# Optimization experiments

Measured on AMD Instinct MI355X. Metric: run time of the kernel, lower is better.

## Reference

```python
import jax, jax.numpy as jnp
import numpy as np

SEQ_LENGTH = 1000
NUM_FEATURES = 5
HIDDEN = 128


def setup_inputs() -> dict:
    key = jax.random.key(0)
    ks = jax.random.split(key, 12)
    k = 1.0 / np.sqrt(HIDDEN)  # torch default uniform bound
    # recurrence stays numerically bounded; math is identical.
    u = lambda kk, shape, s=k: jax.random.uniform(kk, shape, jnp.float32, -s, s)
    return {
        "x": jax.random.normal(ks[0], (256, 800, NUM_FEATURES), jnp.float32),
        "h_state": jnp.zeros((2, 256, HIDDEN), jnp.float32),
        "w_ih0": u(ks[1], (HIDDEN, NUM_FEATURES)),
        "w_hh0": u(ks[2], (HIDDEN, HIDDEN), 0.5 * k),
        "b_ih0": u(ks[3], (HIDDEN,)),
        "b_hh0": u(ks[4], (HIDDEN,)),
        "w_ih1": u(ks[5], (HIDDEN, HIDDEN), 0.5 * k),
        "w_hh1": u(ks[6], (HIDDEN, HIDDEN), 0.5 * k),
        "b_ih1": u(ks[7], (HIDDEN,)),
        "b_hh1": u(ks[8], (HIDDEN,)),
        "w_out": u(ks[9], (1, HIDDEN)),
        "b_out": u(ks[10], (1,)),
    }


def reference(x, h_state, w_ih0, w_hh0, b_ih0, b_hh0,
              w_ih1, w_hh1, b_ih1, b_hh1, w_out, b_out):
    B, T_in, F = x.shape
    # pad time dim to SEQ_LENGTH with zeros (torch.cat with delta)
    pad = jnp.zeros((B, SEQ_LENGTH - T_in, F), x.dtype)
    xp = jnp.concatenate([x, pad], axis=1)  # [B, 1000, F]
    xs = jnp.swapaxes(xp, 0, 1)  # [T, B, F] for scan

    def step(carry, x_t):
        h0, h1 = carry
        h0 = jax.nn.relu(x_t @ w_ih0.T + b_ih0 + h0 @ w_hh0.T + b_hh0)
        h1 = jax.nn.relu(h0 @ w_ih1.T + b_ih1 + h1 @ w_hh1.T + b_hh1)
        return (h0, h1), h1

    (h0f, h1f), ys = jax.lax.scan(step, (h_state[0], h_state[1]), xs)
    r_out = jnp.swapaxes(ys, 0, 1)  # [B, 1000, H]
    out = jax.nn.sigmoid(r_out @ w_out.T + b_out)  # [B, 1000, 1]
    return out[:, :T_in], jnp.stack([h0f, h1f])
```

## Files before the change

### kernel.cpp

```cpp
#include <hip/hip_runtime.h>
#include <math.h>


#define TT    1000
#define TIN   800
#define HD    128
#define NF    5
#define BATCH 256
#define RS    136
#define AS    132
#define SK1   20
#define NSTEP (TT + SK1)

typedef _Float16 h16x2 __attribute__((ext_vector_type(2)));
typedef _Float16 h16x8 __attribute__((ext_vector_type(8)));
typedef float    f32x4 __attribute__((ext_vector_type(4)));

template<int CTRL>
__device__ __forceinline__ float dpp_mov(float v) {
    union { float f; int i; } u, r;
    u.f = v;
    r.i = __builtin_amdgcn_update_dpp(0, u.i, CTRL, 0xF, 0xF, true);
    return r.f;
}

__global__ __launch_bounds__(512, 2) void rnn_dec(
    const float* __restrict__ x,
    const float* __restrict__ h_state,
    const float* __restrict__ w_ih0,
    const float* __restrict__ w_hh0,
    const float* __restrict__ b_ih0,
    const float* __restrict__ b_hh0,
    const float* __restrict__ w_ih1,
    const float* __restrict__ w_hh1,
    const float* __restrict__ b_ih1,
    const float* __restrict__ b_hh1,
    const float* __restrict__ w_out,
    const float* __restrict__ b_out,
    float* __restrict__ out)
{
    __shared__ __align__(16) _Float16 x_h[TIN * 8];
    __shared__ __align__(16) _Float16 ring0[32][RS];
    __shared__ __align__(16) _Float16 ring1[32][RS];
    __shared__ __align__(16) float    A_f[32][AS];
    __shared__ float y_lds[TIN];

    const int tid  = threadIdx.x;
    const int bb   = blockIdx.x;
    const int wv   = tid >> 6;
    const int lane = tid & 63;

    for (int i = tid; i < TIN * 8; i += 512) x_h[i] = (_Float16)0.f;
    __syncthreads();
    for (int i = tid; i < TIN * NF; i += 512) {
        int t = i / 5, f = i - 5 * t;
        x_h[t * 8 + f] = (_Float16)x[bb * (TIN * NF) + i];
    }
    if (tid < HD) {
        ring0[31][tid] = (_Float16)h_state[bb * HD + tid];
        ring1[31][tid] = (_Float16)h_state[BATCH * HD + bb * HD + tid];
    }

    const int c    = lane & 3;
    const int rg   = lane >> 2;
    const int g    = 2 * (c & 1) + ((c >> 1) & 1);
    const int half = wv & 1;
    const int row  = half * 64 + rg * 4 + g;

    union WU {
        h16x2 wp[4][16];
        h16x8 af[4][4];
        h16x2 wo[16];
    } W;

    float bias = 0.f;
    h16x2 wx[3];
    if (wv < 4) {
        const float* Wsrc = (wv < 2) ? w_hh0 : w_hh1;
        #pragma unroll
        for (int j = 0; j < 4; ++j) {
            const float* rp = Wsrc + (half * 64 + rg * 4 + (j ^ g)) * HD + c * 32;
            #pragma unroll
            for (int t = 0; t < 16; ++t) {
                h16x2 w2 = { (_Float16)rp[2 * t], (_Float16)rp[2 * t + 1] };
                W.wp[j][t] = w2;
            }
        }
        if (wv < 2) {
            wx[0][0] = (_Float16)w_ih0[row * NF + 0];
            wx[0][1] = (_Float16)w_ih0[row * NF + 1];
            wx[1][0] = (_Float16)w_ih0[row * NF + 2];
            wx[1][1] = (_Float16)w_ih0[row * NF + 3];
            wx[2][0] = (_Float16)w_ih0[row * NF + 4];
            wx[2][1] = (_Float16)0.f;
            bias = b_ih0[row] + b_hh0[row];
        } else {
            bias = b_ih1[row] + b_hh1[row];
        }
    } else if (wv < 6) {
        const int m0 = (wv - 4) * 64;
        #pragma unroll
        for (int mt = 0; mt < 4; ++mt) {
            #pragma unroll
            for (int kt = 0; kt < 4; ++kt) {
                const float* rp = w_ih1 + (m0 + mt * 16 + (lane & 15)) * HD
                                + kt * 32 + (lane >> 4) * 8;
                h16x8 v;
                #pragma unroll
                for (int j = 0; j < 8; ++j) v[j] = (_Float16)rp[j];
                W.af[mt][kt] = v;
            }
        }
    } else if (wv == 6) {
        const int c4 = lane & 3;
        #pragma unroll
        for (int t = 0; t < 16; ++t) {
            h16x2 w2 = { (_Float16)w_out[c4 * 32 + 2 * t],
                         (_Float16)w_out[c4 * 32 + 2 * t + 1] };
            W.wo[t] = w2;
        }
    }
    const float bout = b_out[0];

    float hfin = 0.f;

    __syncthreads();

    auto matvec = [&](const _Float16* base) -> float {
        h16x8 hv[4];
        #pragma unroll
        for (int u2 = 0; u2 < 4; ++u2)
            hv[u2] = *(const h16x8*)(base + c * 32 + 8 * u2);
        float a[4] = {0.f, 0.f, 0.f, 0.f};
        #pragma unroll
        for (int j = 0; j < 4; ++j) {
            float aj = 0.f;
            #pragma unroll
            for (int t = 0; t < 16; ++t) {
                h16x2 hp = { hv[t >> 2][2 * (t & 3)], hv[t >> 2][2 * (t & 3) + 1] };
                aj = __builtin_amdgcn_fdot2(W.wp[j][t], hp, aj, false);
            }
            a[j] = aj;
        }
        a[0] += dpp_mov<0xB1>(a[2]);
        a[1] += dpp_mov<0xB1>(a[3]);
        a[0] += dpp_mov<0x4E>(a[1]);
        return a[0];
    };

    for (int s = 0; s < NSTEP; ++s) {
        if (wv < 2) {
            if (s < TT) {
                float v = matvec(&ring0[(s + 31) & 31][0]) + bias;
                if (s < TIN) {
                    h16x8 xv = *(const h16x8*)(&x_h[s * 8]);
                    h16x2 xp0 = { xv[0], xv[1] };
                    h16x2 xp1 = { xv[2], xv[3] };
                    h16x2 xp2 = { xv[4], xv[5] };
                    float xc = __builtin_amdgcn_fdot2(wx[2], xp2, 0.f, false);
                    xc = __builtin_amdgcn_fdot2(wx[1], xp1, xc, false);
                    xc = __builtin_amdgcn_fdot2(wx[0], xp0, xc, false);
                    v += xc;
                }
                v = fmaxf(v, 0.f);
                ring0[s & 31][row] = (_Float16)v;
                if (s == TT - 1) hfin = v;
            }
        } else if (wv < 4) {
            if (s >= SK1) {
                const int u = s - SK1;
                float v = matvec(&ring1[(u + 31) & 31][0]);
                v = fmaxf(v + bias + A_f[u & 31][row], 0.f);
                ring1[u & 31][row] = (_Float16)v;
                if (u == TT - 1) hfin = v;
            }
        } else if (wv < 6) {
            if (s >= 17 && s <= 1009 && ((s - 17) & 15) == 0) {
                const int ub = s - 17;
                const int un = ub + (lane & 15);
                h16x8 bf[4];
                #pragma unroll
                for (int kt = 0; kt < 4; ++kt)
                    bf[kt] = *(const h16x8*)(&ring0[un & 31]
                                             [kt * 32 + (lane >> 4) * 8]);
                #pragma unroll
                for (int mt = 0; mt < 4; ++mt) {
                    f32x4 acc = {0.f, 0.f, 0.f, 0.f};
                    #pragma unroll
                    for (int kt = 0; kt < 4; ++kt)
                        acc = __builtin_amdgcn_mfma_f32_16x16x32_f16(
                            W.af[mt][kt], bf[kt], acc, 0, 0, 0);
                    if (un < TT)
                        *(f32x4*)(&A_f[un & 31]
                                  [(wv - 4) * 64 + mt * 16 + (lane >> 4) * 4]) = acc;
                }
            }
        } else if (wv == 6) {
            if (s >= 37 && s <= 821 && ((s - 37) & 15) == 0) {
                const int slot = lane >> 2;
                const int c4   = lane & 3;
                const int t    = (s - 37) + slot;
                const _Float16* rb = &ring1[t & 31][0] + c4 * 32;
                float z = 0.f;
                #pragma unroll
                for (int u2 = 0; u2 < 4; ++u2) {
                    h16x8 hv = *(const h16x8*)(rb + 8 * u2);
                    h16x2 hp0 = { hv[0], hv[1] };
                    h16x2 hp1 = { hv[2], hv[3] };
                    h16x2 hp2 = { hv[4], hv[5] };
                    h16x2 hp3 = { hv[6], hv[7] };
                    z = __builtin_amdgcn_fdot2(W.wo[4 * u2 + 0], hp0, z, false);
                    z = __builtin_amdgcn_fdot2(W.wo[4 * u2 + 1], hp1, z, false);
                    z = __builtin_amdgcn_fdot2(W.wo[4 * u2 + 2], hp2, z, false);
                    z = __builtin_amdgcn_fdot2(W.wo[4 * u2 + 3], hp3, z, false);
                }
                z += dpp_mov<0xB1>(z);
                z += dpp_mov<0x4E>(z);
                if (c4 == 0) y_lds[t] = 1.f / (1.f + expf(-(z + bout)));
            }
        }
        __syncthreads();
    }

    for (int i = tid; i < TIN; i += 512)
        out[bb * TIN + i] = y_lds[i];
    if (wv < 2)
        out[TIN * BATCH + bb * HD + row] = hfin;
    else if (wv < 4)
        out[TIN * BATCH + BATCH * HD + bb * HD + row] = hfin;
}

extern "C" void kernel_launch(void* const* d_in, const int* in_sizes, int n_in,
                              void* d_out, int out_size, void* d_ws, size_t ws_size,
                              hipStream_t stream) {
    (void)in_sizes; (void)n_in; (void)d_ws; (void)ws_size; (void)out_size;
    rnn_dec<<<dim3(BATCH), dim3(512), 0, stream>>>(
        (const float*)d_in[0],  (const float*)d_in[1],
        (const float*)d_in[2],  (const float*)d_in[3],
        (const float*)d_in[4],  (const float*)d_in[5],
        (const float*)d_in[6],  (const float*)d_in[7],
        (const float*)d_in[8],  (const float*)d_in[9],
        (const float*)d_in[10], (const float*)d_in[11],
        (float*)d_out);
}
```

Measured before the change: 429.4 us.

## Halve block to four waves, one per layer, with two steps per barrier

The block shrinks from 512 to 256 threads. Each recurrent layer is now handled by a single wave, with every lane computing two hidden rows over a 64-wide slice, and the MFMA and output-projection waves are merged into the remaining two. The time loop runs two recurrence steps between barriers, relying on in-order LDS access within a wave, to cut barrier count and cross-wave reduction shuffles. In exchange, each step's serial dot-product chain per wave doubles, the wave-level parallelism per CU drops, and the looser synchronisation narrows the margin on ring-buffer reuse.

```diff
diff --git a/kernel.cpp b/kernel.cpp
--- a/kernel.cpp
+++ b/kernel.cpp
@@ -24,7 +24,7 @@
     return r.f;
 }
 
-__global__ __launch_bounds__(512, 2) void rnn_dec(
+__global__ __launch_bounds__(256, 1) void rnn_sc(
     const float* __restrict__ x,
     const float* __restrict__ h_state,
     const float* __restrict__ w_ih0,
@@ -50,9 +50,9 @@
     const int wv   = tid >> 6;
     const int lane = tid & 63;
 
-    for (int i = tid; i < TIN * 8; i += 512) x_h[i] = (_Float16)0.f;
+    for (int i = tid; i < TIN * 8; i += 256) x_h[i] = (_Float16)0.f;
     __syncthreads();
-    for (int i = tid; i < TIN * NF; i += 512) {
+    for (int i = tid; i < TIN * NF; i += 256) {
         int t = i / 5, f = i - 5 * t;
         x_h[t * 8 + f] = (_Float16)x[bb * (TIN * NF) + i];
     }
@@ -61,44 +61,48 @@
         ring1[31][tid] = (_Float16)h_state[BATCH * HD + bb * HD + tid];
     }
 
-    const int c    = lane & 3;
-    const int rg   = lane >> 2;
-    const int g    = 2 * (c & 1) + ((c >> 1) & 1);
-    const int half = wv & 1;
-    const int row  = half * 64 + rg * 4 + g;
+    const int c      = lane & 1;
+    const int rg     = lane >> 1;
+    const int g2     = 2 * c;
+    const int base_r = rg * 4 + 2 * c;
 
     union WU {
-        h16x2 wp[4][16];
+        h16x2 wp[4][32];
         h16x8 af[4][4];
-        h16x2 wo[16];
     } W;
-
-    float bias = 0.f;
-    h16x2 wx[3];
-    if (wv < 4) {
-        const float* Wsrc = (wv < 2) ? w_hh0 : w_hh1;
+    h16x2 wo[16];
+    h16x2 wxa[3], wxb[3];
+    float bias0 = 0.f, bias1 = 0.f;
+
+    if (wv < 2) {
+        const float* Wsrc = (wv == 0) ? w_hh0 : w_hh1;
         #pragma unroll
         for (int j = 0; j < 4; ++j) {
-            const float* rp = Wsrc + (half * 64 + rg * 4 + (j ^ g)) * HD + c * 32;
-            #pragma unroll
-            for (int t = 0; t < 16; ++t) {
+            const float* rp = Wsrc + (rg * 4 + (j ^ g2)) * HD + c * 64;
+            #pragma unroll
+            for (int t = 0; t < 32; ++t) {
                 h16x2 w2 = { (_Float16)rp[2 * t], (_Float16)rp[2 * t + 1] };
                 W.wp[j][t] = w2;
             }
         }
-        if (wv < 2) {
-            wx[0][0] = (_Float16)w_ih0[row * NF + 0];
-            wx[0][1] = (_Float16)w_ih0[row * NF + 1];
-            wx[1][0] = (_Float16)w_ih0[row * NF + 2];
-            wx[1][1] = (_Float16)w_ih0[row * NF + 3];
-            wx[2][0] = (_Float16)w_ih0[row * NF + 4];
-            wx[2][1] = (_Float16)0.f;
-            bias = b_ih0[row] + b_hh0[row];
+        if (wv == 0) {
+            #pragma unroll
+            for (int k = 0; k < 3; ++k) {
+                _Float16 a0 = (_Float16)w_ih0[base_r * NF + 2 * k];
+                _Float16 a1 = (2 * k + 1 < NF) ? (_Float16)w_ih0[base_r * NF + 2 * k + 1] : (_Float16)0.f;
+                _Float16 b0 = (_Float16)w_ih0[(base_r + 1) * NF + 2 * k];
+                _Float16 b1 = (2 * k + 1 < NF) ? (_Float16)w_ih0[(base_r + 1) * NF + 2 * k + 1] : (_Float16)0.f;
+                h16x2 wa = { a0, a1 }; wxa[k] = wa;
+                h16x2 wb = { b0, b1 }; wxb[k] = wb;
+            }
+            bias0 = b_ih0[base_r] + b_hh0[base_r];
+            bias1 = b_ih0[base_r + 1] + b_hh0[base_r + 1];
         } else {
-            bias = b_ih1[row] + b_hh1[row];
-        }
-    } else if (wv < 6) {
-        const int m0 = (wv - 4) * 64;
+            bias0 = b_ih1[base_r] + b_hh1[base_r];
+            bias1 = b_ih1[base_r + 1] + b_hh1[base_r + 1];
+        }
+    } else {
+        const int m0 = (wv == 2) ? 0 : 64;
         #pragma unroll
         for (int mt = 0; mt < 4; ++mt) {
             #pragma unroll
@@ -111,32 +115,33 @@
                 W.af[mt][kt] = v;
             }
         }
-    } else if (wv == 6) {
-        const int c4 = lane & 3;
-        #pragma unroll
-        for (int t = 0; t < 16; ++t) {
-            h16x2 w2 = { (_Float16)w_out[c4 * 32 + 2 * t],
-                         (_Float16)w_out[c4 * 32 + 2 * t + 1] };
-            W.wo[t] = w2;
+        if (wv == 3) {
+            const int c4 = lane & 3;
+            #pragma unroll
+            for (int t = 0; t < 16; ++t) {
+                h16x2 w2 = { (_Float16)w_out[c4 * 32 + 2 * t],
+                             (_Float16)w_out[c4 * 32 + 2 * t + 1] };
+                wo[t] = w2;
+            }
         }
     }
     const float bout = b_out[0];
 
-    float hfin = 0.f;
+    float hfin0 = 0.f, hfin1 = 0.f;
 
     __syncthreads();
 
-    auto matvec = [&](const _Float16* base) -> float {
-        h16x8 hv[4];
-        #pragma unroll
-        for (int u2 = 0; u2 < 4; ++u2)
-            hv[u2] = *(const h16x8*)(base + c * 32 + 8 * u2);
+    auto matvec = [&](const _Float16* base, float& r0, float& r1) {
+        h16x8 hv[8];
+        #pragma unroll
+        for (int u2 = 0; u2 < 8; ++u2)
+            hv[u2] = *(const h16x8*)(base + c * 64 + 8 * u2);
         float a[4] = {0.f, 0.f, 0.f, 0.f};
         #pragma unroll
         for (int j = 0; j < 4; ++j) {
             float aj = 0.f;
             #pragma unroll
-            for (int t = 0; t < 16; ++t) {
+            for (int t = 0; t < 32; ++t) {
                 h16x2 hp = { hv[t >> 2][2 * (t & 3)], hv[t >> 2][2 * (t & 3) + 1] };
                 aj = __builtin_amdgcn_fdot2(W.wp[j][t], hp, aj, false);
             }
@@ -144,38 +149,50 @@
         }
         a[0] += dpp_mov<0xB1>(a[2]);
         a[1] += dpp_mov<0xB1>(a[3]);
-        a[0] += dpp_mov<0x4E>(a[1]);
-        return a[0];
+        r0 = a[0];
+        r1 = a[1];
     };
 
-    for (int s = 0; s < NSTEP; ++s) {
-        if (wv < 2) {
+    auto body = [&](int s) {
+        if (wv == 0) {
             if (s < TT) {
-                float v = matvec(&ring0[(s + 31) & 31][0]) + bias;
+                float v0, v1;
+                matvec(&ring0[(s + 31) & 31][0], v0, v1);
+                v0 += bias0; v1 += bias1;
                 if (s < TIN) {
                     h16x8 xv = *(const h16x8*)(&x_h[s * 8]);
                     h16x2 xp0 = { xv[0], xv[1] };
                     h16x2 xp1 = { xv[2], xv[3] };
                     h16x2 xp2 = { xv[4], xv[5] };
-                    float xc = __builtin_amdgcn_fdot2(wx[2], xp2, 0.f, false);
-                    xc = __builtin_amdgcn_fdot2(wx[1], xp1, xc, false);
-                    xc = __builtin_amdgcn_fdot2(wx[0], xp0, xc, false);
-                    v += xc;
+                    float xc0 = __builtin_amdgcn_fdot2(wxa[2], xp2, 0.f, false);
+                    xc0 = __builtin_amdgcn_fdot2(wxa[1], xp1, xc0, false);
+                    xc0 = __builtin_amdgcn_fdot2(wxa[0], xp0, xc0, false);
+                    float xc1 = __builtin_amdgcn_fdot2(wxb[2], xp2, 0.f, false);
+                    xc1 = __builtin_amdgcn_fdot2(wxb[1], xp1, xc1, false);
+                    xc1 = __builtin_amdgcn_fdot2(wxb[0], xp0, xc1, false);
+                    v0 += xc0; v1 += xc1;
                 }
-                v = fmaxf(v, 0.f);
-                ring0[s & 31][row] = (_Float16)v;
-                if (s == TT - 1) hfin = v;
-            }
-        } else if (wv < 4) {
+                v0 = fmaxf(v0, 0.f);
+                v1 = fmaxf(v1, 0.f);
+                h16x2 hv = { (_Float16)v0, (_Float16)v1 };
+                *(h16x2*)(&ring0[s & 31][base_r]) = hv;
+                if (s == TT - 1) { hfin0 = v0; hfin1 = v1; }
+            }
+        } else if (wv == 1) {
             if (s >= SK1) {
                 const int u = s - SK1;
-                float v = matvec(&ring1[(u + 31) & 31][0]);
-                v = fmaxf(v + bias + A_f[u & 31][row], 0.f);
-                ring1[u & 31][row] = (_Float16)v;
-                if (u == TT - 1) hfin = v;
-            }
-        } else if (wv < 6) {
+                float v0, v1;
+                matvec(&ring1[(u + 31) & 31][0], v0, v1);
+                float2 av = *(const float2*)(&A_f[u & 31][base_r]);
+                v0 = fmaxf(v0 + bias0 + av.x, 0.f);
+                v1 = fmaxf(v1 + bias1 + av.y, 0.f);
+                h16x2 hv = { (_Float16)v0, (_Float16)v1 };
+                *(h16x2*)(&ring1[u & 31][base_r]) = hv;
+                if (u == TT - 1) { hfin0 = v0; hfin1 = v1; }
+            }
+        } else {
             if (s >= 17 && s <= 1009 && ((s - 17) & 15) == 0) {
+                const int m0 = (wv == 2) ? 0 : 64;
                 const int ub = s - 17;
                 const int un = ub + (lane & 15);
                 h16x8 bf[4];
@@ -192,11 +209,10 @@
                             W.af[mt][kt], bf[kt], acc, 0, 0, 0);
                     if (un < TT)
                         *(f32x4*)(&A_f[un & 31]
-                                  [(wv - 4) * 64 + mt * 16 + (lane >> 4) * 4]) = acc;
+                                  [m0 + mt * 16 + (lane >> 4) * 4]) = acc;
                 }
             }
-        } else if (wv == 6) {
-            if (s >= 37 && s <= 821 && ((s - 37) & 15) == 0) {
+            if (wv == 3 && s >= 37 && s <= 821 && ((s - 37) & 15) == 0) {
                 const int slot = lane >> 2;
                 const int c4   = lane & 3;
                 const int t    = (s - 37) + slot;
@@ -209,32 +225,37 @@
                     h16x2 hp1 = { hv[2], hv[3] };
                     h16x2 hp2 = { hv[4], hv[5] };
                     h16x2 hp3 = { hv[6], hv[7] };
-                    z = __builtin_amdgcn_fdot2(W.wo[4 * u2 + 0], hp0, z, false);
-                    z = __builtin_amdgcn_fdot2(W.wo[4 * u2 + 1], hp1, z, false);
-                    z = __builtin_amdgcn_fdot2(W.wo[4 * u2 + 2], hp2, z, false);
-                    z = __builtin_amdgcn_fdot2(W.wo[4 * u2 + 3], hp3, z, false);
+                    z = __builtin_amdgcn_fdot2(wo[4 * u2 + 0], hp0, z, false);
+                    z = __builtin_amdgcn_fdot2(wo[4 * u2 + 1], hp1, z, false);
+                    z = __builtin_amdgcn_fdot2(wo[4 * u2 + 2], hp2, z, false);
+                    z = __builtin_amdgcn_fdot2(wo[4 * u2 + 3], hp3, z, false);
                 }
                 z += dpp_mov<0xB1>(z);
                 z += dpp_mov<0x4E>(z);
                 if (c4 == 0) y_lds[t] = 1.f / (1.f + expf(-(z + bout)));
             }
         }
+    };
+
+    for (int s2 = 0; s2 < NSTEP; s2 += 2) {
+        body(s2);
+        body(s2 + 1);
         __syncthreads();
     }
 
-    for (int i = tid; i < TIN; i += 512)
+    for (int i = tid; i < TIN; i += 256)
         out[bb * TIN + i] = y_lds[i];
-    if (wv < 2)
-        out[TIN * BATCH + bb * HD + row] = hfin;
-    else if (wv < 4)
-        out[TIN * BATCH + BATCH * HD + bb * HD + row] = hfin;
+    if (wv == 0)
+        *(float2*)(&out[TIN * BATCH + bb * HD + base_r]) = make_float2(hfin0, hfin1);
+    else if (wv == 1)
+        *(float2*)(&out[TIN * BATCH + BATCH * HD + bb * HD + base_r]) = make_float2(hfin0, hfin1);
 }
 
 extern "C" void kernel_launch(void* const* d_in, const int* in_sizes, int n_in,
                               void* d_out, int out_size, void* d_ws, size_t ws_size,
                               hipStream_t stream) {
     (void)in_sizes; (void)n_in; (void)d_ws; (void)ws_size; (void)out_size;
-    rnn_dec<<<dim3(BATCH), dim3(512), 0, stream>>>(
+    rnn_sc<<<dim3(BATCH), dim3(256), 0, stream>>>(
         (const float*)d_in[0],  (const float*)d_in[1],
         (const float*)d_in[2],  (const float*)d_in[3],
         (const float*)d_in[4],  (const float*)d_in[5],
```

After: 517.3 us. +20.5%, slower.

## Shrink block to six waves and precompute layer-0 input projection in bursts

Applied to the files above, without the earlier changes.

Block size drops from eight waves to six (one idle wave was already unused). The output-projection work moves onto MFMA wave 4, and wave 5 computes the layer-0 input contribution for 16 timesteps at a time into a new LDS ring. Layer-0 waves then do a single LDS read on the critical path instead of three fdot2 ops. The per-step barrier involves fewer waves, which should cut sync cost. The trade-offs are extra LDS, more work on the MFMA waves, and a launch bound of one block per SIMD set.

```diff
diff --git a/kernel.cpp b/kernel.cpp
--- a/kernel.cpp
+++ b/kernel.cpp
@@ -24,7 +24,7 @@
     return r.f;
 }
 
-__global__ __launch_bounds__(512, 2) void rnn_dec(
+__global__ __launch_bounds__(384, 1) void rnn_c6(
     const float* __restrict__ x,
     const float* __restrict__ h_state,
     const float* __restrict__ w_ih0,
@@ -43,6 +43,7 @@
     __shared__ __align__(16) _Float16 ring0[32][RS];
     __shared__ __align__(16) _Float16 ring1[32][RS];
     __shared__ __align__(16) float    A_f[32][AS];
+    __shared__ __align__(16) float    xc_f[32][AS];
     __shared__ float y_lds[TIN];
 
     const int tid  = threadIdx.x;
@@ -50,9 +51,9 @@
     const int wv   = tid >> 6;
     const int lane = tid & 63;
 
-    for (int i = tid; i < TIN * 8; i += 512) x_h[i] = (_Float16)0.f;
+    for (int i = tid; i < TIN * 8; i += 384) x_h[i] = (_Float16)0.f;
     __syncthreads();
-    for (int i = tid; i < TIN * NF; i += 512) {
+    for (int i = tid; i < TIN * NF; i += 384) {
         int t = i / 5, f = i - 5 * t;
         x_h[t * 8 + f] = (_Float16)x[bb * (TIN * NF) + i];
     }
@@ -70,11 +71,11 @@
     union WU {
         h16x2 wp[4][16];
         h16x8 af[4][4];
-        h16x2 wo[16];
     } W;
-
+    h16x2 wo[16];
+    h16x2 xwa[3], xwb[3];
     float bias = 0.f;
-    h16x2 wx[3];
+
     if (wv < 4) {
         const float* Wsrc = (wv < 2) ? w_hh0 : w_hh1;
         #pragma unroll
@@ -86,19 +87,10 @@
                 W.wp[j][t] = w2;
             }
         }
-        if (wv < 2) {
-            wx[0][0] = (_Float16)w_ih0[row * NF + 0];
-            wx[0][1] = (_Float16)w_ih0[row * NF + 1];
-            wx[1][0] = (_Float16)w_ih0[row * NF + 2];
-            wx[1][1] = (_Float16)w_ih0[row * NF + 3];
-            wx[2][0] = (_Float16)w_ih0[row * NF + 4];
-            wx[2][1] = (_Float16)0.f;
-            bias = b_ih0[row] + b_hh0[row];
-        } else {
-            bias = b_ih1[row] + b_hh1[row];
-        }
-    } else if (wv < 6) {
-        const int m0 = (wv - 4) * 64;
+        bias = (wv < 2) ? (b_ih0[row] + b_hh0[row])
+                        : (b_ih1[row] + b_hh1[row]);
+    } else {
+        const int m0 = (wv == 4) ? 0 : 64;
         #pragma unroll
         for (int mt = 0; mt < 4; ++mt) {
             #pragma unroll
@@ -111,19 +103,51 @@
                 W.af[mt][kt] = v;
             }
         }
-    } else if (wv == 6) {
-        const int c4 = lane & 3;
-        #pragma unroll
-        for (int t = 0; t < 16; ++t) {
-            h16x2 w2 = { (_Float16)w_out[c4 * 32 + 2 * t],
-                         (_Float16)w_out[c4 * 32 + 2 * t + 1] };
-            W.wo[t] = w2;
+        if (wv == 4) {
+            const int c4 = lane & 3;
+            #pragma unroll
+            for (int t = 0; t < 16; ++t) {
+                h16x2 w2 = { (_Float16)w_out[c4 * 32 + 2 * t],
+                             (_Float16)w_out[c4 * 32 + 2 * t + 1] };
+                wo[t] = w2;
+            }
+        } else {
+            #pragma unroll
+            for (int k = 0; k < 3; ++k) {
+                _Float16 a0 = (_Float16)w_ih0[(2 * lane) * NF + 2 * k];
+                _Float16 a1 = (2 * k + 1 < NF) ? (_Float16)w_ih0[(2 * lane) * NF + 2 * k + 1] : (_Float16)0.f;
+                _Float16 b0 = (_Float16)w_ih0[(2 * lane + 1) * NF + 2 * k];
+                _Float16 b1 = (2 * k + 1 < NF) ? (_Float16)w_ih0[(2 * lane + 1) * NF + 2 * k + 1] : (_Float16)0.f;
+                h16x2 wa = { a0, a1 }; xwa[k] = wa;
+                h16x2 wb = { b0, b1 }; xwb[k] = wb;
+            }
         }
     }
     const float bout = b_out[0];
 
     float hfin = 0.f;
 
+    __syncthreads();
+
+    auto xc_burst = [&](int tb) {
+        #pragma unroll
+        for (int ti = 0; ti < 16; ++ti) {
+            const int t = tb + ti;
+            h16x8 xv = *(const h16x8*)(&x_h[t * 8]);
+            h16x2 xp0 = { xv[0], xv[1] };
+            h16x2 xp1 = { xv[2], xv[3] };
+            h16x2 xp2 = { xv[4], xv[5] };
+            float c0 = __builtin_amdgcn_fdot2(xwa[2], xp2, 0.f, false);
+            c0 = __builtin_amdgcn_fdot2(xwa[1], xp1, c0, false);
+            c0 = __builtin_amdgcn_fdot2(xwa[0], xp0, c0, false);
+            float c1 = __builtin_amdgcn_fdot2(xwb[2], xp2, 0.f, false);
+            c1 = __builtin_amdgcn_fdot2(xwb[1], xp1, c1, false);
+            c1 = __builtin_amdgcn_fdot2(xwb[0], xp0, c1, false);
+            *(float2*)(&xc_f[t & 31][2 * lane]) = make_float2(c0, c1);
+        }
+    };
+
+    if (wv == 5) xc_burst(0);
     __syncthreads();
 
     auto matvec = [&](const _Float16* base) -> float {
@@ -152,16 +176,7 @@
         if (wv < 2) {
             if (s < TT) {
                 float v = matvec(&ring0[(s + 31) & 31][0]) + bias;
-                if (s < TIN) {
-                    h16x8 xv = *(const h16x8*)(&x_h[s * 8]);
-                    h16x2 xp0 = { xv[0], xv[1] };
-                    h16x2 xp1 = { xv[2], xv[3] };
-                    h16x2 xp2 = { xv[4], xv[5] };
-                    float xc = __builtin_amdgcn_fdot2(wx[2], xp2, 0.f, false);
-                    xc = __builtin_amdgcn_fdot2(wx[1], xp1, xc, false);
-                    xc = __builtin_amdgcn_fdot2(wx[0], xp0, xc, false);
-                    v += xc;
-                }
+                if (s < TIN) v += xc_f[s & 31][row];
                 v = fmaxf(v, 0.f);
                 ring0[s & 31][row] = (_Float16)v;
                 if (s == TT - 1) hfin = v;
@@ -174,8 +189,9 @@
                 ring1[u & 31][row] = (_Float16)v;
                 if (u == TT - 1) hfin = v;
             }
-        } else if (wv < 6) {
+        } else {
             if (s >= 17 && s <= 1009 && ((s - 17) & 15) == 0) {
+                const int m0 = (wv == 4) ? 0 : 64;
                 const int ub = s - 17;
                 const int un = ub + (lane & 15);
                 h16x8 bf[4];
@@ -192,37 +208,42 @@
                             W.af[mt][kt], bf[kt], acc, 0, 0, 0);
                     if (un < TT)
                         *(f32x4*)(&A_f[un & 31]
-                                  [(wv - 4) * 64 + mt * 16 + (lane >> 4) * 4]) = acc;
+                                  [m0 + mt * 16 + (lane >> 4) * 4]) = acc;
                 }
             }
-        } else if (wv == 6) {
-            if (s >= 37 && s <= 821 && ((s - 37) & 15) == 0) {
-                const int slot = lane >> 2;
-                const int c4   = lane & 3;
-                const int t    = (s - 37) + slot;
-                const _Float16* rb = &ring1[t & 31][0] + c4 * 32;
-                float z = 0.f;
-                #pragma unroll
-                for (int u2 = 0; u2 < 4; ++u2) {
-                    h16x8 hv = *(const h16x8*)(rb + 8 * u2);
-                    h16x2 hp0 = { hv[0], hv[1] };
-                    h16x2 hp1 = { hv[2], hv[3] };
-                    h16x2 hp2 = { hv[4], hv[5] };
-                    h16x2 hp3 = { hv[6], hv[7] };
-                    z = __builtin_amdgcn_fdot2(W.wo[4 * u2 + 0], hp0, z, false);
-                    z = __builtin_amdgcn_fdot2(W.wo[4 * u2 + 1], hp1, z, false);
-                    z = __builtin_amdgcn_fdot2(W.wo[4 * u2 + 2], hp2, z, false);
-                    z = __builtin_amdgcn_fdot2(W.wo[4 * u2 + 3], hp3, z, false);
+            if (wv == 4) {
+                if (s >= 37 && s <= 821 && ((s - 37) & 15) == 0) {
+                    const int slot = lane >> 2;
+                    const int c4   = lane & 3;
+                    const int t    = (s - 37) + slot;
+                    const _Float16* rb = &ring1[t & 31][0] + c4 * 32;
+                    float z = 0.f;
+                    #pragma unroll
+                    for (int u2 = 0; u2 < 4; ++u2) {
+                        h16x8 hv = *(const h16x8*)(rb + 8 * u2);
+                        h16x2 hp0 = { hv[0], hv[1] };
+                        h16x2 hp1 = { hv[2], hv[3] };
+                        h16x2 hp2 = { hv[4], hv[5] };
+                        h16x2 hp3 = { hv[6], hv[7] };
+                        z = __builtin_amdgcn_fdot2(wo[4 * u2 + 0], hp0, z, false);
+                        z = __builtin_amdgcn_fdot2(wo[4 * u2 + 1], hp1, z, false);
+                        z = __builtin_amdgcn_fdot2(wo[4 * u2 + 2], hp2, z, false);
+                        z = __builtin_amdgcn_fdot2(wo[4 * u2 + 3], hp3, z, false);
+                    }
+                    z += dpp_mov<0xB1>(z);
+                    z += dpp_mov<0x4E>(z);
+                    if (c4 == 0) y_lds[t] = 1.f / (1.f + expf(-(z + bout)));
                 }
-                z += dpp_mov<0xB1>(z);
-                z += dpp_mov<0x4E>(z);
-                if (c4 == 0) y_lds[t] = 1.f / (1.f + expf(-(z + bout)));
+            } else {
+                if (s >= 9 && s <= 777 && ((s - 9) & 15) == 0) {
+                    xc_burst(s + 7);
+                }
             }
         }
         __syncthreads();
     }
 
-    for (int i = tid; i < TIN; i += 512)
+    for (int i = tid; i < TIN; i += 384)
         out[bb * TIN + i] = y_lds[i];
     if (wv < 2)
         out[TIN * BATCH + bb * HD + row] = hfin;
@@ -234,7 +255,7 @@
                               void* d_out, int out_size, void* d_ws, size_t ws_size,
                               hipStream_t stream) {
     (void)in_sizes; (void)n_in; (void)d_ws; (void)ws_size; (void)out_size;
-    rnn_dec<<<dim3(BATCH), dim3(512), 0, stream>>>(
+    rnn_c6<<<dim3(BATCH), dim3(384), 0, stream>>>(
         (const float*)d_in[0],  (const float*)d_in[1],
         (const float*)d_in[2],  (const float*)d_in[3],
         (const float*)d_in[4],  (const float*)d_in[5],
```

After: 428.8 us. About the same (-0.1%).
